# Kernel optimization log

Measured on AMD Instinct MI355X. Metric: run time of the kernel, lower is better.

The kernel has to match this reference:

```python
import jax, jax.numpy as jnp
import numpy as np

B, C, H, W, K = 2, 36, 512, 512, 9
GROUPS, GSIZE = 3, 12  # channel groups 0:12, 12:24, 24:36


def _grid_sample_bilinear(feat, gx, gy):
    """Bilinear grid_sample, align_corners=True. feat [B,C,H,W]; gx,gy [B,H,W] in [-1,1]."""
    Bn, Cn, Hn, Wn = feat.shape
    px = (gx + 1.0) * 0.5 * (Wn - 1)
    py = (gy + 1.0) * 0.5 * (Hn - 1)
    x0 = jnp.floor(px)
    y0 = jnp.floor(py)
    wx = (px - x0)[:, None, :, :]
    wy = (py - y0)[:, None, :, :]
    x0i = jnp.clip(x0.astype(jnp.int32), 0, Wn - 1)
    x1i = jnp.clip(x0i + 1, 0, Wn - 1)
    y0i = jnp.clip(y0.astype(jnp.int32), 0, Hn - 1)
    y1i = jnpip = jnp.clip(y0.astype(jnp.int32) + 1, 0, Hn - 1)
    flat = feat.reshape(Bn, Cn, Hn * Wn)
    gather = jax.vmap(lambda f, yi, xi: f[:, yi * Wn + xi])  # -> [B,C,H,W]
    v00 = gather(flat, y0i, x0i)
    v01 = gather(flat, y0i, x1i)
    v10 = gather(flat, y1i, x0i)
    v11 = gather(flat, y1i, x1i)
    return (v00 * (1 - wx) * (1 - wy) + v01 * wx * (1 - wy)
            + v10 * (1 - wx) * wy + v11 * wx * wy)


def setup_inputs() -> dict:
    key = jax.random.key(0)
    k1, k2, k3 = jax.random.split(key, 3)
    features = jax.random.normal(k1, (B, C, H, W), jnp.float32)
    offset_x = jax.random.normal(k2, (B, K, H, W), jnp.float32) * 16.0
    offset_y = jax.random.normal(k3, (B, K, H, W), jnp.float32) * 16.0
    left_x = jnp.broadcast_to(jnp.arange(W, dtype=jnp.float32)[None, None, None, :], (B, 1, H, W))
    left_y = jnp.broadcast_to(jnp.arange(H, dtype=jnp.float32)[None, None, :, None], (B, 1, H, W))
    return {"features": features, "offset_x": offset_x, "offset_y": offset_y,
            "left_x": jnp.array(left_x), "left_y": jnp.array(left_y)}


def reference(features, offset_x, offset_y, left_x, left_y):
    Hn, Wn = features.shape[2], features.shape[3]
    # clamp candidate coords to image, then normalize to [-1,1]
    rx = jnp.clip(left_x + offset_x, 0.0, Wn - 1)
    ry = jnp.clip(left_y + offset_y, 0.0, Hn - 1)
    gx = (rx - (Wn - 1) / 2.0) / ((Wn - 1) / 2.0)  # [B,K,H,W]
    gy = (ry - (Hn - 1) / 2.0) / ((Hn - 1) / 2.0)

    def per_candidate(g):
        gxk, gyk = g  # each [B,H,W]
        a = _grid_sample_bilinear(features, gxk, gyk)  # [B,36,H,W]
        a2 = jnp.roll(a, 12, axis=1)
        a3 = jnp.roll(a, 24, axis=1)

        def grp_mean(d):  # [B,36,H,W] -> [B,3,H,W] mean over 12-channel groups
            return d.reshape(d.shape[0], GROUPS, GSIZE, d.shape[2], d.shape[3]).mean(axis=2)

        s = jnp.concatenate([grp_mean(-jnp.abs(features - a)),
                             grp_mean(-jnp.abs(features - a2)),
                             grp_mean(-jnp.abs(features - a3))], axis=1)  # [B,9,H,W]
        return jnp.max(s, axis=1)  # top-1 of sort == max  -> [B,H,W]

    strengths = jax.lax.map(per_candidate,
                            (jnp.moveaxis(gx, 1, 0), jnp.moveaxis(gy, 1, 0)))  # [K,B,H,W]
    strengths = jnp.moveaxis(strengths, 0, 1)  # [B,K,H,W]

    wgt = jax.nn.softmax(strengths * 1000.0, axis=1)
    ox = jnp.sum(offset_x * wgt, axis=1, keepdims=True)
    oy = jnp.sum(offset_y * wgt, axis=1, keepdims=True)
    oy = jnp.clip(oy + left_y, 0.0, Hn - 1) - left_y
    ox = jnp.clip(ox + left_x, 0.0, Wn - 1) - left_x
    return ox, oy
```

## Files before the change

kernel.cpp:

```cpp
#include <hip/hip_runtime.h>
#include <math.h>

#define B_ 2
#define C_ 36
#define H_ 512
#define W_ 512
#define K_ 9
#define HW_ (H_ * W_)
#define ROWF4 (W_ * C_ / 4)

__global__ __launch_bounds__(256) void transpose_kernel(const float* __restrict__ in,
                                                        float* __restrict__ out) {
  __shared__ float tile[64][37];
  int blk = blockIdx.x;
  int wt = blk & 7;
  int h = (blk >> 3) & (H_ - 1);
  int b = blk >> 12;
  int w0 = wt << 6;
  int tid = threadIdx.x;
  const float* src = in + ((size_t)b * C_) * HW_ + (size_t)h * W_ + w0;
#pragma unroll
  for (int it = 0; it < 9; ++it) {
    int idx = it * 256 + tid;
    int c = idx >> 6;
    int wl = idx & 63;
    tile[wl][c] = src[(size_t)c * HW_ + wl];
  }
  __syncthreads();
  float* dst = out + (((size_t)b * H_ + h) * W_ + w0) * C_;
#pragma unroll
  for (int it = 0; it < 9; ++it) {
    int idx = it * 256 + tid;
    int wl = idx / 36;
    int c = idx - wl * 36;
    dst[idx] = tile[wl][c];
  }
}

__global__ __launch_bounds__(64, 2) void eval_kernel_cw(const float* __restrict__ feat,
                                                        const float* __restrict__ offx,
                                                        const float* __restrict__ offy,
                                                        float* __restrict__ out) {
  __shared__ __align__(16) float scratch[32 * 36];
  __shared__ __align__(16) float4 w_lds[64];
  __shared__ int a_lds[64];

  int tid = threadIdx.x;
  int blk = blockIdx.x;
  int region = blk & 7;
  int slot = blk >> 3;
  int b = region >> 2;
  int qd = region & 3;
  int qy = (qd >> 1) << 8;
  int qx = (qd & 1) << 8;
  int tr = slot >> 5;
  int tc = slot & 31;
  if (tr & 1) tc = 31 - tc;
  int h = qy + tr * 8 + (tid >> 3);
  int w = qx + tc * 8 + (tid & 7);
  int ph = h * W_ + w;
  int p = b * HW_ + ph;

  const float4* feat4 = reinterpret_cast<const float4*>(feat);

  const float* oxb = offx + (size_t)b * K_ * HW_ + ph;
  const float* oyb = offy + (size_t)b * K_ * HW_ + ph;
  float oxv[K_], oyv[K_];
#pragma unroll
  for (int k = 0; k < K_; ++k) {
    oxv[k] = oxb[k * HW_];
    oyv[k] = oyb[k * HW_];
  }

  float F[C_];
  {
    const float4* myF = feat4 + (size_t)p * 9;
#pragma unroll
    for (int i = 0; i < 9; ++i) {
      float4 v = myF[i];
      F[4 * i + 0] = v.x; F[4 * i + 1] = v.y; F[4 * i + 2] = v.z; F[4 * i + 3] = v.w;
    }
  }

  int g = tid / 9;
  int q = tid - 9 * g;

  float lx = (float)w;
  float ly = (float)h;

  float M = -INFINITY, den = 0.f, axs = 0.f, ays = 0.f;

#pragma unroll 1
  for (int k = 0; k < K_; ++k) {
    float ox = oxv[k];
    float oy = oyv[k];
    float rx = fminf(fmaxf(lx + ox, 0.0f), 511.0f);
    float ry = fminf(fmaxf(ly + oy, 0.0f), 511.0f);
    float gx = (rx - 255.5f) / 255.5f;
    float gy = (ry - 255.5f) / 255.5f;
    float px = (gx + 1.0f) * 0.5f * 511.0f;
    float py = (gy + 1.0f) * 0.5f * 511.0f;
    int x0 = (int)floorf(px); x0 = (x0 > 510) ? 510 : x0;
    int y0 = (int)floorf(py); y0 = (y0 > 510) ? 510 : y0;
    float wx = px - (float)x0;
    float wy = py - (float)y0;
    w_lds[tid] = make_float4((1.0f - wx) * (1.0f - wy), wx * (1.0f - wy),
                             (1.0f - wx) * wy, wx * wy);
    a_lds[tid] = ((b * H_ + y0) * W_ + x0) * 9;
    __syncthreads();

    float4 L[5][4];
#pragma unroll
    for (int r = 0; r < 5; ++r) {
      int tt = 7 * r + g;
      int t = (tt > 31) ? 31 : tt;
      const float4* r0 = feat4 + a_lds[t];
      L[r][0] = r0[q];
      L[r][1] = r0[9 + q];
      L[r][2] = r0[ROWF4 + q];
      L[r][3] = r0[ROWF4 + 9 + q];
    }
#pragma unroll
    for (int r = 0; r < 5; ++r) {
      int tt = 7 * r + g;
      int t = (tt > 31) ? 31 : tt;
      float4 W4 = w_lds[t];
      float4 v00 = L[r][0], v01 = L[r][1], v10 = L[r][2], v11 = L[r][3];
      float4 a4;
      a4.x = W4.x * v00.x + W4.y * v01.x + W4.z * v10.x + W4.w * v11.x;
      a4.y = W4.x * v00.y + W4.y * v01.y + W4.z * v10.y + W4.w * v11.y;
      a4.z = W4.x * v00.z + W4.y * v01.z + W4.z * v10.z + W4.w * v11.z;
      a4.w = W4.x * v00.w + W4.y * v01.w + W4.z * v10.w + W4.w * v11.w;
      if (tt < 32 && tid < 63) {
        *reinterpret_cast<float4*>(&scratch[t * 36 + 4 * q]) = a4;
      }
    }
#pragma unroll
    for (int r = 0; r < 5; ++r) {
      int tt = 32 + 7 * r + g;
      int t = (tt > 63) ? 63 : tt;
      const float4* r0 = feat4 + a_lds[t];
      L[r][0] = r0[q];
      L[r][1] = r0[9 + q];
      L[r][2] = r0[ROWF4 + q];
      L[r][3] = r0[ROWF4 + 9 + q];
    }
    if (tid < 32) {
      float D[9] = {0.f, 0.f, 0.f, 0.f, 0.f, 0.f, 0.f, 0.f, 0.f};
      const float4* sc = reinterpret_cast<const float4*>(&scratch[tid * 36]);
#pragma unroll
      for (int q2 = 0; q2 < 9; ++q2) {
        float4 a4 = sc[q2];
        float av[4] = {a4.x, a4.y, a4.z, a4.w};
        int ga = q2 / 3;
        int f0 = 4 * (q2 % 3);
#pragma unroll
        for (int j = 0; j < 4; ++j) {
          D[ga]     += fabsf(F[f0 + j]      - av[j]);
          D[3 + ga] += fabsf(F[12 + f0 + j] - av[j]);
          D[6 + ga] += fabsf(F[24 + f0 + j] - av[j]);
        }
      }
      float mn = D[0];
#pragma unroll
      for (int j = 1; j < 9; ++j) mn = fminf(mn, D[j]);
      float xk = -(mn / 12.0f) * 1000.0f;
      float nm = fmaxf(M, xk);
      float scl = expf(M - nm);
      float ek = expf(xk - nm);
      den = den * scl + ek;
      axs = axs * scl + ox * ek;
      ays = ays * scl + oy * ek;
      M = nm;
    }
#pragma unroll
    for (int r = 0; r < 5; ++r) {
      int tt = 32 + 7 * r + g;
      int t = (tt > 63) ? 63 : tt;
      float4 W4 = w_lds[t];
      float4 v00 = L[r][0], v01 = L[r][1], v10 = L[r][2], v11 = L[r][3];
      float4 a4;
      a4.x = W4.x * v00.x + W4.y * v01.x + W4.z * v10.x + W4.w * v11.x;
      a4.y = W4.x * v00.y + W4.y * v01.y + W4.z * v10.y + W4.w * v11.y;
      a4.z = W4.x * v00.z + W4.y * v01.z + W4.z * v10.z + W4.w * v11.z;
      a4.w = W4.x * v00.w + W4.y * v01.w + W4.z * v10.w + W4.w * v11.w;
      if (tt < 64 && tid < 63) {
        *reinterpret_cast<float4*>(&scratch[(t - 32) * 36 + 4 * q]) = a4;
      }
    }
    if (tid >= 32) {
      float D[9] = {0.f, 0.f, 0.f, 0.f, 0.f, 0.f, 0.f, 0.f, 0.f};
      const float4* sc = reinterpret_cast<const float4*>(&scratch[(tid - 32) * 36]);
#pragma unroll
      for (int q2 = 0; q2 < 9; ++q2) {
        float4 a4 = sc[q2];
        float av[4] = {a4.x, a4.y, a4.z, a4.w};
        int ga = q2 / 3;
        int f0 = 4 * (q2 % 3);
#pragma unroll
        for (int j = 0; j < 4; ++j) {
          D[ga]     += fabsf(F[f0 + j]      - av[j]);
          D[3 + ga] += fabsf(F[12 + f0 + j] - av[j]);
          D[6 + ga] += fabsf(F[24 + f0 + j] - av[j]);
        }
      }
      float mn = D[0];
#pragma unroll
      for (int j = 1; j < 9; ++j) mn = fminf(mn, D[j]);
      float xk = -(mn / 12.0f) * 1000.0f;
      float nm = fmaxf(M, xk);
      float scl = expf(M - nm);
      float ek = expf(xk - nm);
      den = den * scl + ek;
      axs = axs * scl + ox * ek;
      ays = ays * scl + oy * ek;
      M = nm;
    }
  }

  float resx = axs / den;
  float resy = ays / den;
  out[p] = fminf(fmaxf(resx + lx, 0.0f), 511.0f) - lx;
  out[B_ * HW_ + p] = fminf(fmaxf(resy + ly, 0.0f), 511.0f) - ly;
}

__global__ __launch_bounds__(256) void eval_kernel_n(const float* __restrict__ feat,
                                                     const float* __restrict__ offx,
                                                     const float* __restrict__ offy,
                                                     float* __restrict__ out) {
  int p = blockIdx.x * 256 + threadIdx.x;
  int ph = p & (HW_ - 1);
  int b = p >> 18;
  float F[C_];
  const float* fb = feat + (size_t)b * C_ * HW_ + ph;
#pragma unroll
  for (int c = 0; c < C_; ++c) F[c] = fb[(size_t)c * HW_];
  float lx = (float)(ph & (W_ - 1));
  float ly = (float)((ph >> 9) & (H_ - 1));
  const float* oxb = offx + (size_t)b * K_ * HW_ + ph;
  const float* oyb = offy + (size_t)b * K_ * HW_ + ph;
  float M = -INFINITY, den = 0.f, ax = 0.f, ay = 0.f;
#pragma unroll 1
  for (int k = 0; k < K_; ++k) {
    float ox = oxb[k * HW_];
    float oy = oyb[k * HW_];
    float rx = fminf(fmaxf(lx + ox, 0.0f), 511.0f);
    float ry = fminf(fmaxf(ly + oy, 0.0f), 511.0f);
    float gx = (rx - 255.5f) / 255.5f;
    float gy = (ry - 255.5f) / 255.5f;
    float px = (gx + 1.0f) * 0.5f * 511.0f;
    float py = (gy + 1.0f) * 0.5f * 511.0f;
    int x0 = (int)floorf(px); x0 = (x0 > 510) ? 510 : x0;
    int y0 = (int)floorf(py); y0 = (y0 > 510) ? 510 : y0;
    float wx = px - (float)x0;
    float wy = py - (float)y0;
    float w00 = (1.0f - wx) * (1.0f - wy);
    float w01 = wx * (1.0f - wy);
    float w10 = (1.0f - wx) * wy;
    float w11 = wx * wy;
    float D[9] = {0.f, 0.f, 0.f, 0.f, 0.f, 0.f, 0.f, 0.f, 0.f};
    const float* pl = feat + (size_t)b * C_ * HW_ + (size_t)y0 * W_ + x0;
#pragma unroll
    for (int c = 0; c < C_; ++c) {
      const float* q0 = pl + (size_t)c * HW_;
      float v00 = q0[0], v01 = q0[1];
      float v10 = q0[W_], v11 = q0[W_ + 1];
      float a = v00 * w00 + v01 * w01 + v10 * w10 + v11 * w11;
      int i = c % 12;
      int ga = c / 12;
      D[ga]     += fabsf(F[i]      - a);
      D[3 + ga] += fabsf(F[12 + i] - a);
      D[6 + ga] += fabsf(F[24 + i] - a);
    }
    float mn = D[0];
#pragma unroll
    for (int j = 1; j < 9; ++j) mn = fminf(mn, D[j]);
    float xk = -(mn / 12.0f) * 1000.0f;
    float nm = fmaxf(M, xk);
    float sc = expf(M - nm);
    float ek = expf(xk - nm);
    den = den * sc + ek;
    ax = ax * sc + ox * ek;
    ay = ay * sc + oy * ek;
    M = nm;
  }
  float resx = ax / den;
  float resy = ay / den;
  out[p] = fminf(fmaxf(resx + lx, 0.0f), 511.0f) - lx;
  out[B_ * HW_ + p] = fminf(fmaxf(resy + ly, 0.0f), 511.0f) - ly;
}

extern "C" void kernel_launch(void* const* d_in, const int* in_sizes, int n_in,
                              void* d_out, int out_size, void* d_ws, size_t ws_size,
                              hipStream_t stream) {
  const float* features = (const float*)d_in[0];
  const float* offset_x = (const float*)d_in[1];
  const float* offset_y = (const float*)d_in[2];
  float* out = (float*)d_out;

  const int npix = B_ * HW_;
  const size_t need = (size_t)npix * C_ * sizeof(float);

  if (ws_size >= need) {
    float* featT = (float*)d_ws;
    transpose_kernel<<<B_ * H_ * (W_ / 64), 256, 0, stream>>>(features, featT);
    eval_kernel_cw<<<npix / 64, 64, 0, stream>>>(featT, offset_x, offset_y, out);
  } else {
    eval_kernel_n<<<npix / 256, 256, 0, stream>>>(features, offset_x, offset_y, out);
  }
}
```

Before: 313.5 us.

## Pack four wavefronts per block as 16x16 tiles and load offsets lazily

Changes the eval kernel from one 64-thread wave per block to 256-thread blocks of four independent waves, each covering an 8x8 sub-tile of a 16x16 pixel tile with its own private LDS slice. Launch bounds move to 256 threads with a minimum of 3 blocks per CU. The per-pixel offset preload into 18 registers is replaced by a per-iteration global load, which cuts register pressure to help occupancy at the cost of load latency inside the loop. The __syncthreads calls now synchronize all four waves even though each wave only uses its own LDS slice, adding unneeded barrier coupling.

```diff
diff --git a/kernel.cpp b/kernel.cpp
--- a/kernel.cpp
+++ b/kernel.cpp
@@ -37,15 +37,17 @@
   }
 }
 
-__global__ __launch_bounds__(64, 2) void eval_kernel_cw(const float* __restrict__ feat,
-                                                        const float* __restrict__ offx,
-                                                        const float* __restrict__ offy,
-                                                        float* __restrict__ out) {
-  __shared__ __align__(16) float scratch[32 * 36];
-  __shared__ __align__(16) float4 w_lds[64];
-  __shared__ int a_lds[64];
+__global__ __launch_bounds__(256, 3) void eval_kernel_cw(const float* __restrict__ feat,
+                                                         const float* __restrict__ offx,
+                                                         const float* __restrict__ offy,
+                                                         float* __restrict__ out) {
+  __shared__ __align__(16) float scratch[4][32 * 36];
+  __shared__ __align__(16) float4 w_lds[4][64];
+  __shared__ int a_lds[4][64];
 
   int tid = threadIdx.x;
+  int wv = tid >> 6;
+  int lane = tid & 63;
   int blk = blockIdx.x;
   int region = blk & 7;
   int slot = blk >> 3;
@@ -53,24 +55,23 @@
   int qd = region & 3;
   int qy = (qd >> 1) << 8;
   int qx = (qd & 1) << 8;
-  int tr = slot >> 5;
-  int tc = slot & 31;
-  if (tr & 1) tc = 31 - tc;
-  int h = qy + tr * 8 + (tid >> 3);
-  int w = qx + tc * 8 + (tid & 7);
+  int tr = slot >> 4;
+  int tc = slot & 15;
+  if (tr & 1) tc = 15 - tc;
+  int sy = (wv >> 1) << 3;
+  int sx = (wv & 1) << 3;
+  int h = qy + tr * 16 + sy + (lane >> 3);
+  int w = qx + tc * 16 + sx + (lane & 7);
   int ph = h * W_ + w;
   int p = b * HW_ + ph;
 
   const float4* feat4 = reinterpret_cast<const float4*>(feat);
+  float* scr = scratch[wv];
+  float4* wl_ = w_lds[wv];
+  int* al_ = a_lds[wv];
 
   const float* oxb = offx + (size_t)b * K_ * HW_ + ph;
   const float* oyb = offy + (size_t)b * K_ * HW_ + ph;
-  float oxv[K_], oyv[K_];
-#pragma unroll
-  for (int k = 0; k < K_; ++k) {
-    oxv[k] = oxb[k * HW_];
-    oyv[k] = oyb[k * HW_];
-  }
 
   float F[C_];
   {
@@ -82,8 +83,8 @@
     }
   }
 
-  int g = tid / 9;
-  int q = tid - 9 * g;
+  int g = lane / 9;
+  int q = lane - 9 * g;
 
   float lx = (float)w;
   float ly = (float)h;
@@ -92,8 +93,8 @@
 
 #pragma unroll 1
   for (int k = 0; k < K_; ++k) {
-    float ox = oxv[k];
-    float oy = oyv[k];
+    float ox = oxb[k * HW_];
+    float oy = oyb[k * HW_];
     float rx = fminf(fmaxf(lx + ox, 0.0f), 511.0f);
     float ry = fminf(fmaxf(ly + oy, 0.0f), 511.0f);
     float gx = (rx - 255.5f) / 255.5f;
@@ -104,9 +105,9 @@
     int y0 = (int)floorf(py); y0 = (y0 > 510) ? 510 : y0;
     float wx = px - (float)x0;
     float wy = py - (float)y0;
-    w_lds[tid] = make_float4((1.0f - wx) * (1.0f - wy), wx * (1.0f - wy),
-                             (1.0f - wx) * wy, wx * wy);
-    a_lds[tid] = ((b * H_ + y0) * W_ + x0) * 9;
+    wl_[lane] = make_float4((1.0f - wx) * (1.0f - wy), wx * (1.0f - wy),
+                            (1.0f - wx) * wy, wx * wy);
+    al_[lane] = ((b * H_ + y0) * W_ + x0) * 9;
     __syncthreads();
 
     float4 L[5][4];
@@ -114,7 +115,7 @@
     for (int r = 0; r < 5; ++r) {
       int tt = 7 * r + g;
       int t = (tt > 31) ? 31 : tt;
-      const float4* r0 = feat4 + a_lds[t];
+      const float4* r0 = feat4 + al_[t];
       L[r][0] = r0[q];
       L[r][1] = r0[9 + q];
       L[r][2] = r0[ROWF4 + q];
@@ -124,30 +125,30 @@
     for (int r = 0; r < 5; ++r) {
       int tt = 7 * r + g;
       int t = (tt > 31) ? 31 : tt;
-      float4 W4 = w_lds[t];
+      float4 W4 = wl_[t];
       float4 v00 = L[r][0], v01 = L[r][1], v10 = L[r][2], v11 = L[r][3];
       float4 a4;
       a4.x = W4.x * v00.x + W4.y * v01.x + W4.z * v10.x + W4.w * v11.x;
       a4.y = W4.x * v00.y + W4.y * v01.y + W4.z * v10.y + W4.w * v11.y;
       a4.z = W4.x * v00.z + W4.y * v01.z + W4.z * v10.z + W4.w * v11.z;
       a4.w = W4.x * v00.w + W4.y * v01.w + W4.z * v10.w + W4.w * v11.w;
-      if (tt < 32 && tid < 63) {
-        *reinterpret_cast<float4*>(&scratch[t * 36 + 4 * q]) = a4;
+      if (tt < 32 && lane < 63) {
+        *reinterpret_cast<float4*>(&scr[t * 36 + 4 * q]) = a4;
       }
     }
 #pragma unroll
     for (int r = 0; r < 5; ++r) {
       int tt = 32 + 7 * r + g;
       int t = (tt > 63) ? 63 : tt;
-      const float4* r0 = feat4 + a_lds[t];
+      const float4* r0 = feat4 + al_[t];
       L[r][0] = r0[q];
       L[r][1] = r0[9 + q];
       L[r][2] = r0[ROWF4 + q];
       L[r][3] = r0[ROWF4 + 9 + q];
     }
-    if (tid < 32) {
+    if (lane < 32) {
       float D[9] = {0.f, 0.f, 0.f, 0.f, 0.f, 0.f, 0.f, 0.f, 0.f};
-      const float4* sc = reinterpret_cast<const float4*>(&scratch[tid * 36]);
+      const float4* sc = reinterpret_cast<const float4*>(&scr[lane * 36]);
 #pragma unroll
       for (int q2 = 0; q2 < 9; ++q2) {
         float4 a4 = sc[q2];
@@ -177,20 +178,20 @@
     for (int r = 0; r < 5; ++r) {
       int tt = 32 + 7 * r + g;
       int t = (tt > 63) ? 63 : tt;
-      float4 W4 = w_lds[t];
+      float4 W4 = wl_[t];
       float4 v00 = L[r][0], v01 = L[r][1], v10 = L[r][2], v11 = L[r][3];
       float4 a4;
       a4.x = W4.x * v00.x + W4.y * v01.x + W4.z * v10.x + W4.w * v11.x;
       a4.y = W4.x * v00.y + W4.y * v01.y + W4.z * v10.y + W4.w * v11.y;
       a4.z = W4.x * v00.z + W4.y * v01.z + W4.z * v10.z + W4.w * v11.z;
       a4.w = W4.x * v00.w + W4.y * v01.w + W4.z * v10.w + W4.w * v11.w;
-      if (tt < 64 && tid < 63) {
-        *reinterpret_cast<float4*>(&scratch[(t - 32) * 36 + 4 * q]) = a4;
+      if (tt < 64 && lane < 63) {
+        *reinterpret_cast<float4*>(&scr[(t - 32) * 36 + 4 * q]) = a4;
       }
     }
-    if (tid >= 32) {
+    if (lane >= 32) {
       float D[9] = {0.f, 0.f, 0.f, 0.f, 0.f, 0.f, 0.f, 0.f, 0.f};
-      const float4* sc = reinterpret_cast<const float4*>(&scratch[(tid - 32) * 36]);
+      const float4* sc = reinterpret_cast<const float4*>(&scr[(lane - 32) * 36]);
 #pragma unroll
       for (int q2 = 0; q2 < 9; ++q2) {
         float4 a4 = sc[q2];
@@ -304,7 +305,7 @@
   if (ws_size >= need) {
     float* featT = (float*)d_ws;
     transpose_kernel<<<B_ * H_ * (W_ / 64), 256, 0, stream>>>(features, featT);
-    eval_kernel_cw<<<npix / 64, 64, 0, stream>>>(featT, offset_x, offset_y, out);
+    eval_kernel_cw<<<npix / 256, 256, 0, stream>>>(featT, offset_x, offset_y, out);
   } else {
     eval_kernel_n<<<npix / 256, 256, 0, stream>>>(features, offset_x, offset_y, out);
   }
```

After: 332.3 us. 1.06x slower.
